# Kernel tuning notes

Measured on AMD Instinct MI355X. Metric: run time of the kernel, lower is better.

## Reference

```python
import jax, jax.numpy as jnp
import numpy as np

VOCAB = 32000
EMB = 1024
BLOCK = 2048
B = 4


def setup_inputs() -> dict:
    key = jax.random.key(0)
    ks = jax.random.split(key, 10)
    s = EMB ** -0.5
    return {
        "idx": jax.random.randint(ks[0], (B, BLOCK), 0, VOCAB),
        "targets": jax.random.randint(ks[1], (B, BLOCK), 0, VOCAB),
        "tok_emb": jax.random.normal(ks[2], (VOCAB, EMB), jnp.float32),
        "pos_emb": jax.random.normal(ks[3], (BLOCK, EMB), jnp.float32),
        "Wk": jax.random.normal(ks[4], (EMB, EMB), jnp.float32) * s,
        "Wq": jax.random.normal(ks[5], (EMB, EMB), jnp.float32) * s,
        "Wv": jax.random.normal(ks[6], (EMB, EMB), jnp.float32) * s,
        "Wlm": jax.random.normal(ks[7], (EMB, VOCAB), jnp.float32) * s,
        "blm": jnp.zeros((VOCAB,), jnp.float32),
    }


def reference(idx, targets, tok_emb, pos_emb, Wk, Wq, Wv, Wlm, blm):
    B_, T = idx.shape
    x = tok_emb[idx] + pos_emb[:T]  # [B,T,C]
    C = x.shape[-1]
    k = x @ Wk  # [B,T,H]
    q = x @ Wq
    v = x @ Wv
    wei = jnp.einsum("bth,bsh->bts", q, k) * (C ** -0.5)  # [B,T,T]
    causal = jnp.tril(jnp.ones((T, T), bool))
    wei = jnp.where(causal, wei, -jnp.inf)
    wei = jax.nn.softmax(wei, axis=-1)
    out = jnp.einsum("bts,bsh->bth", wei, v)  # [B,T,H]
    logits = out @ Wlm + blm  # [B,T,V]
    logits2d = logits.reshape(B_ * T, -1)
    tgt = targets.reshape(B_ * T)
    logp = jax.nn.log_softmax(logits2d, axis=-1)
    loss = -jnp.mean(jnp.take_along_axis(logp, tgt[:, None], axis=1))
    return logits2d, loss
```

## Files before the change

### kernel.cpp

```cpp
#include <hip/hip_runtime.h>
#include <hip/hip_bf16.h>
#include <cstdint>

#define VOCAB 32000
#define EMB   1024
#define TLEN  2048
#define NB    4
#define MTOT  (NB*TLEN)

typedef __bf16 bf16;
typedef __bf16 bf16x8 __attribute__((ext_vector_type(8)));
typedef float  f32x4  __attribute__((ext_vector_type(4)));

__global__ void embed_kernel(const int* __restrict__ idx,
                             const float* __restrict__ tok,
                             const float* __restrict__ pos,
                             bf16* __restrict__ x)
{
    int gid = blockIdx.x * 256 + threadIdx.x;
    int r   = gid >> 7;
    int c0  = (gid & 127) << 3;
    int t   = r & (TLEN - 1);
    int tk  = idx[r];
    const float4* tp = reinterpret_cast<const float4*>(tok + (long)tk * EMB + c0);
    const float4* pp = reinterpret_cast<const float4*>(pos + (long)t  * EMB + c0);
    float4 a0 = tp[0], a1 = tp[1];
    float4 b0 = pp[0], b1 = pp[1];
    bf16x8 o;
    o[0] = (bf16)(a0.x + b0.x); o[1] = (bf16)(a0.y + b0.y);
    o[2] = (bf16)(a0.z + b0.z); o[3] = (bf16)(a0.w + b0.w);
    o[4] = (bf16)(a1.x + b1.x); o[5] = (bf16)(a1.y + b1.y);
    o[6] = (bf16)(a1.z + b1.z); o[7] = (bf16)(a1.w + b1.w);
    *reinterpret_cast<bf16x8*>(x + (long)r * EMB + c0) = o;
}

__global__ void transpose_conv_kernel(const float* __restrict__ W,
                                      bf16* __restrict__ Wt,
                                      int Kdim, int Ndim)
{
    __shared__ bf16 tile[64][65];
    int n0 = blockIdx.x * 64;
    int k0 = blockIdx.y * 64;
    int tid = threadIdx.x;
    int c  = tid & 63, r0 = tid >> 6;
#pragma unroll
    for (int i = 0; i < 16; ++i) {
        int r = r0 + i * 4;
        tile[r][c] = (bf16)W[(long)(k0 + r) * Ndim + n0 + c];
    }
    __syncthreads();
    int kc = tid & 63, nr0 = tid >> 6;
#pragma unroll
    for (int i = 0; i < 16; ++i) {
        int nr = nr0 + i * 4;
        Wt[(long)(n0 + nr) * Kdim + k0 + kc] = tile[kc][nr];
    }
}

__device__ __forceinline__ void gll16(const void* g, void* l)
{
    __builtin_amdgcn_global_load_lds(
        (const __attribute__((address_space(1))) unsigned int*)g,
        (__attribute__((address_space(3))) unsigned int*)l, 16, 0, 0);
}

__device__ __forceinline__ void stage256s(const bf16* __restrict__ gbase,
                                          int ld, int kt, bf16* lbase, int tid)
{
#pragma unroll
    for (int p = 0; p < 4; ++p) {
        int lin  = p * 512 + tid;
        int row  = lin >> 3;
        int slot = lin & 7;
        int ke   = ((slot ^ (row & 7)) << 3) + kt;
        gll16(gbase + (long)row * ld + ke, lbase + lin * 8);
    }
}

template<int CMODE>
__global__ __launch_bounds__(512)
void gemm256_bt(const bf16* __restrict__ A, int lda, long sA,
                const bf16* __restrict__ Bt, int ldb, long sB,
                bf16* __restrict__ C, int ldc, long sC, int K)
{
    if (CMODE == 1 && blockIdx.x > blockIdx.y) return;

    extern __shared__ bf16 smem[];
    bf16* As = smem;
    bf16* Bs = smem + 32768;

    const int tid  = threadIdx.x;
    const int lane = tid & 63, wid = tid >> 6;
    const int wr = wid >> 2, wc = wid & 3;
    const int l15 = lane & 15, hi = lane >> 4, l7 = lane & 7;
    const long zb = blockIdx.z;

    const bf16* Ab = A  + zb * sA + (long)(blockIdx.y * 256) * lda;
    const bf16* Bb = Bt + zb * sB + (long)(blockIdx.x * 256) * ldb;

    const int Keff = (CMODE == 2) ? (int)((blockIdx.y + 1) * 256) : K;
    const int NT   = Keff >> 6;

    f32x4 acc[8][4] = {};

    stage256s(Ab, lda, 0, As, tid);
    stage256s(Bb, ldb, 0, Bs, tid);
    __syncthreads();

#pragma unroll 1
    for (int t = 0; t < NT; ++t) {
        const int buf = t & 1;
        if (t + 1 < NT) {
            stage256s(Ab, lda, (t + 1) * 64, As + (buf ^ 1) * 16384, tid);
            stage256s(Bb, ldb, (t + 1) * 64, Bs + (buf ^ 1) * 16384, tid);
        }
        const bf16* Ap = As + buf * 16384 + (wr * 128) * 64;
        const bf16* Bp = Bs + buf * 16384 + (wc * 64) * 64;
#pragma unroll
        for (int ks = 0; ks < 2; ++ks) {
            const int ko = 8 * (((ks << 2) | hi) ^ l7);
            bf16x8 bfr[4];
#pragma unroll
            for (int n = 0; n < 4; ++n)
                bfr[n] = *(const bf16x8*)(Bp + (n * 16 + l15) * 64 + ko);
#pragma unroll
            for (int m = 0; m < 8; ++m) {
                bf16x8 af = *(const bf16x8*)(Ap + (m * 16 + l15) * 64 + ko);
#pragma unroll
                for (int n = 0; n < 4; ++n)
                    acc[m][n] = __builtin_amdgcn_mfma_f32_16x16x32_bf16(
                                    af, bfr[n], acc[m][n], 0, 0, 0);
            }
        }
        __syncthreads();
    }

    bf16* Cb = C + zb * sC;
    const int colb = blockIdx.x * 256 + wc * 64 + l15;
    const int rowb = blockIdx.y * 256 + wr * 128 + (hi << 2);
#pragma unroll
    for (int m = 0; m < 8; ++m)
#pragma unroll
        for (int n = 0; n < 4; ++n)
#pragma unroll
            for (int r = 0; r < 4; ++r)
                Cb[(long)(rowb + m * 16 + r) * ldc + colb + n * 16] =
                    (bf16)acc[m][n][r];
}

__global__ __launch_bounds__(512)
void gemm256_logits(const bf16* __restrict__ A, const bf16* __restrict__ Bt,
                    float* __restrict__ C, const float* __restrict__ bias,
                    float2* __restrict__ part)
{
    extern __shared__ bf16 smem[];
    bf16* As = smem;
    bf16* Bs = smem + 32768;

    const int tid  = threadIdx.x;
    const int lane = tid & 63, wid = tid >> 6;
    const int wr = wid >> 2, wc = wid & 3;
    const int l15 = lane & 15, hi = lane >> 4, l7 = lane & 7;

    const int wg = blockIdx.x;
    const int xcd = wg & 7, c = wg >> 3;
    const int nb = c >> 2;
    const int mb = xcd * 4 + (c & 3);

    const bf16* Ab = A  + (long)(mb * 256) * EMB;
    const bf16* Bb = Bt + (long)(nb * 256) * EMB;

    f32x4 acc[8][4] = {};

    stage256s(Ab, EMB, 0, As, tid);
    stage256s(Bb, EMB, 0, Bs, tid);
    __syncthreads();

    const int NT = EMB / 64;
#pragma unroll 1
    for (int t = 0; t < NT; ++t) {
        const int buf = t & 1;
        if (t + 1 < NT) {
            stage256s(Ab, EMB, (t + 1) * 64, As + (buf ^ 1) * 16384, tid);
            stage256s(Bb, EMB, (t + 1) * 64, Bs + (buf ^ 1) * 16384, tid);
        }
        const bf16* Ap = As + buf * 16384 + (wr * 128) * 64;
        const bf16* Bp = Bs + buf * 16384 + (wc * 64) * 64;
#pragma unroll
        for (int ks = 0; ks < 2; ++ks) {
            const int ko = 8 * (((ks << 2) | hi) ^ l7);
            bf16x8 bfr[4];
#pragma unroll
            for (int n = 0; n < 4; ++n)
                bfr[n] = *(const bf16x8*)(Bp + (n * 16 + l15) * 64 + ko);
#pragma unroll
            for (int m = 0; m < 8; ++m) {
                bf16x8 af = *(const bf16x8*)(Ap + (m * 16 + l15) * 64 + ko);
#pragma unroll
                for (int n = 0; n < 4; ++n)
                    acc[m][n] = __builtin_amdgcn_mfma_f32_16x16x32_bf16(
                                    af, bfr[n], acc[m][n], 0, 0, 0);
            }
        }
        __syncthreads();
    }

    float* pm = (float*)smem;
    float* ps = pm + 1024;

    const long colbase = (long)nb * 256 + wc * 64 + l15;
    float bv[4];
#pragma unroll
    for (int n = 0; n < 4; ++n) bv[n] = bias[colbase + n * 16];

    const long rowbase = (long)mb * 256 + wr * 128;
#pragma unroll
    for (int m = 0; m < 8; ++m) {
#pragma unroll
        for (int r = 0; r < 4; ++r) {
            float v0 = acc[m][0][r] + bv[0];
            float v1 = acc[m][1][r] + bv[1];
            float v2 = acc[m][2][r] + bv[2];
            float v3 = acc[m][3][r] + bv[3];
            long row = rowbase + m * 16 + (hi << 2) + r;
            float* Cp = C + row * (long)VOCAB + colbase;
            __builtin_nontemporal_store(v0, Cp);
            __builtin_nontemporal_store(v1, Cp + 16);
            __builtin_nontemporal_store(v2, Cp + 32);
            __builtin_nontemporal_store(v3, Cp + 48);

            float lm = fmaxf(fmaxf(v0, v1), fmaxf(v2, v3));
#pragma unroll
            for (int o = 1; o < 16; o <<= 1) lm = fmaxf(lm, __shfl_xor(lm, o));
            float sp = __expf(v0 - lm) + __expf(v1 - lm) +
                       __expf(v2 - lm) + __expf(v3 - lm);
#pragma unroll
            for (int o = 1; o < 16; o <<= 1) sp += __shfl_xor(sp, o);
            if (l15 == 0) {
                int rb = wr * 128 + m * 16 + (hi << 2) + r;
                pm[wc * 256 + rb] = lm;
                ps[wc * 256 + rb] = sp;
            }
        }
    }
    __syncthreads();
    if (tid < 256) {
        float m0 = pm[tid], m1 = pm[256 + tid], m2 = pm[512 + tid], m3 = pm[768 + tid];
        float M = fmaxf(fmaxf(m0, m1), fmaxf(m2, m3));
        float S = ps[tid] * __expf(m0 - M) + ps[256 + tid] * __expf(m1 - M) +
                  ps[512 + tid] * __expf(m2 - M) + ps[768 + tid] * __expf(m3 - M);
        part[((long)mb * 256 + tid) * 125 + nb] = make_float2(M, S);
    }
}

__global__ void softmax_causal_kernel(const bf16* __restrict__ S,
                                      bf16* __restrict__ P)
{
    const int r = blockIdx.x;
    const int t = r & (TLEN - 1);
    const int limit = ((t >> 8) + 1) << 8;
    const int tid = threadIdx.x;
    const int lane = tid & 63, wv = tid >> 6;
    const float scale = 0.03125f;
    const int c0 = tid * 8;

    float v[8];
    float m = -1e30f;
    if (c0 < limit) {
        bf16x8 sv = *(const bf16x8*)(S + (long)r * TLEN + c0);
#pragma unroll
        for (int i = 0; i < 8; ++i) {
            float x = (c0 + i <= t) ? (float)sv[i] * scale : -1e30f;
            v[i] = x;
            m = fmaxf(m, x);
        }
    } else {
#pragma unroll
        for (int i = 0; i < 8; ++i) v[i] = -1e30f;
    }
    __shared__ float red[4];
#pragma unroll
    for (int off = 32; off; off >>= 1) m = fmaxf(m, __shfl_xor(m, off));
    if (lane == 0) red[wv] = m;
    __syncthreads();
    m = fmaxf(fmaxf(red[0], red[1]), fmaxf(red[2], red[3]));
    __syncthreads();

    float s = 0.f;
#pragma unroll
    for (int i = 0; i < 8; ++i) { v[i] = __expf(v[i] - m); s += v[i]; }
#pragma unroll
    for (int off = 32; off; off >>= 1) s += __shfl_xor(s, off);
    if (lane == 0) red[wv] = s;
    __syncthreads();
    s = red[0] + red[1] + red[2] + red[3];
    float inv = 1.0f / s;
    if (c0 < limit) {
        bf16x8 o;
#pragma unroll
        for (int i = 0; i < 8; ++i) o[i] = (bf16)(v[i] * inv);
        *(bf16x8*)(P + (long)r * TLEN + c0) = o;
    }
}

__global__ void loss_combine_kernel(const float2* __restrict__ part,
                                    const float* __restrict__ logits,
                                    const int* __restrict__ tgt,
                                    float* __restrict__ bsum)
{
    const int tid = threadIdx.x;
    const int row = blockIdx.x * 256 + tid;
    const int lane = tid & 63, wv = tid >> 6;
    const float2* p = part + (long)row * 125;
    float M = -1e30f, S = 0.f;
    for (int i = 0; i < 125; ++i) {
        float2 v = p[i];
        if (v.x <= M) S += v.y * __expf(v.x - M);
        else { S = S * __expf(M - v.x) + v.y; M = v.x; }
    }
    float lse = M + __logf(S);
    float l = lse - logits[(long)row * VOCAB + tgt[row]];
#pragma unroll
    for (int off = 32; off; off >>= 1) l += __shfl_xor(l, off);
    __shared__ float red[4];
    if (lane == 0) red[wv] = l;
    __syncthreads();
    if (tid == 0) bsum[blockIdx.x] = red[0] + red[1] + red[2] + red[3];
}

__global__ void loss_final_kernel(const float* __restrict__ bsum,
                                  float* __restrict__ out)
{
    const int lane = threadIdx.x;
    float s = (lane < 32) ? bsum[lane] : 0.f;
#pragma unroll
    for (int off = 32; off; off >>= 1) s += __shfl_xor(s, off);
    if (lane == 0) out[0] = s * (1.0f / MTOT);
}

extern "C" void kernel_launch(void* const* d_in, const int* in_sizes, int n_in,
                              void* d_out, int out_size, void* d_ws, size_t ws_size,
                              hipStream_t stream)
{
    const int*   idx = (const int*)  d_in[0];
    const int*   tgt = (const int*)  d_in[1];
    const float* tok = (const float*)d_in[2];
    const float* pos = (const float*)d_in[3];
    const float* Wk  = (const float*)d_in[4];
    const float* Wq  = (const float*)d_in[5];
    const float* Wv  = (const float*)d_in[6];
    const float* Wlm = (const float*)d_in[7];
    const float* blm = (const float*)d_in[8];
    float* out = (float*)d_out;

    char* ws = (char*)d_ws;
    if (ws_size < (size_t)140 * 1024 * 1024) return;

    bf16*   x     = (bf16*)(ws);
    bf16*   qk    = (bf16*)(ws + (16l << 20));
    bf16*   v_t   = (bf16*)(ws + (48l << 20));
    bf16*   S     = (bf16*)(ws + (64l << 20));
    bf16*   Wqk_t = (bf16*)(ws + (96l << 20));
    bf16*   Wv_t  = (bf16*)(ws + (100l << 20));
    bf16*   att   = (bf16*)(ws);
    bf16*   P     = (bf16*)(ws + (16l << 20));
    bf16*   Wlm_t = (bf16*)(ws + (48l << 20));
    float2* part  = (float2*)(ws + (112l << 20));
    float*  bsum  = (float*)(ws + (120l << 20));

    embed_kernel<<<dim3(MTOT * EMB / 8 / 256), 256, 0, stream>>>(idx, tok, pos, x);

    transpose_conv_kernel<<<dim3(16, 16), 256, 0, stream>>>(Wq, Wqk_t, EMB, EMB);
    transpose_conv_kernel<<<dim3(16, 16), 256, 0, stream>>>(Wk, Wqk_t + 1024 * 1024, EMB, EMB);
    transpose_conv_kernel<<<dim3(16, 16), 256, 0, stream>>>(Wv, Wv_t, EMB, EMB);

    gemm256_bt<0><<<dim3(2048 / 256, MTOT / 256, 1), 512, 131072, stream>>>(
        x, EMB, 0, Wqk_t, EMB, 0, qk, 2048, 0, EMB);
    gemm256_bt<0><<<dim3(MTOT / 256, EMB / 256, 1), 512, 131072, stream>>>(
        Wv_t, EMB, 0, x, EMB, 0, v_t, MTOT, 0, EMB);

    gemm256_bt<1><<<dim3(TLEN / 256, TLEN / 256, NB), 512, 131072, stream>>>(
        qk, 2048, (long)TLEN * 2048, qk + 1024, 2048, (long)TLEN * 2048,
        S, TLEN, (long)TLEN * TLEN, EMB);

    softmax_causal_kernel<<<dim3(MTOT), 256, 0, stream>>>(S, P);

    gemm256_bt<2><<<dim3(EMB / 256, TLEN / 256, NB), 512, 131072, stream>>>(
        P, TLEN, (long)TLEN * TLEN, v_t, MTOT, (long)TLEN,
        att, EMB, (long)TLEN * EMB, TLEN);

    transpose_conv_kernel<<<dim3(VOCAB / 64, EMB / 64), 256, 0, stream>>>(
        Wlm, Wlm_t, EMB, VOCAB);

    gemm256_logits<<<dim3(4000), 512, 131072, stream>>>(att, Wlm_t, out, blm, part);

    loss_combine_kernel<<<dim3(32), 256, 0, stream>>>(part, out, tgt, bsum);
    loss_final_kernel<<<dim3(1), 64, 0, stream>>>(bsum, out + (long)MTOT * VOCAB);
}
```

Before: 847.2 us.

## Co-schedule independent GEMMs and Wlm transpose in combined launches

Merges the V projection GEMM with the causal QK^T score GEMM into one launch, indexing only the lower-triangle tiles directly instead of launching and early-exiting the upper ones. Also merges the causal P·V GEMM with the Wlm transpose/convert into one launch, so the memory-bound transpose blocks fill compute units left idle by the small GEMM grid. Workspace offsets move so Wlm_t no longer aliases v_t while both are live. The cost is branchy heterogeneous blocks that all reserve 128KB of LDS, which limits occupancy for the transpose blocks.

```diff
diff --git a/kernel.cpp b/kernel.cpp
--- a/kernel.cpp
+++ b/kernel.cpp
@@ -78,27 +78,23 @@
 }
 
 template<int CMODE>
-__global__ __launch_bounds__(512)
-void gemm256_bt(const bf16* __restrict__ A, int lda, long sA,
-                const bf16* __restrict__ Bt, int ldb, long sB,
-                bf16* __restrict__ C, int ldc, long sC, int K)
-{
-    if (CMODE == 1 && blockIdx.x > blockIdx.y) return;
-
-    extern __shared__ bf16 smem[];
+__device__ __forceinline__ void gemm256_body(
+    const bf16* __restrict__ A, int lda, long sA,
+    const bf16* __restrict__ Bt, int ldb, long sB,
+    bf16* __restrict__ C, int ldc, long sC, int K,
+    int bx, int by, int zb, bf16* smem, int tid)
+{
     bf16* As = smem;
     bf16* Bs = smem + 32768;
 
-    const int tid  = threadIdx.x;
     const int lane = tid & 63, wid = tid >> 6;
     const int wr = wid >> 2, wc = wid & 3;
     const int l15 = lane & 15, hi = lane >> 4, l7 = lane & 7;
-    const long zb = blockIdx.z;
-
-    const bf16* Ab = A  + zb * sA + (long)(blockIdx.y * 256) * lda;
-    const bf16* Bb = Bt + zb * sB + (long)(blockIdx.x * 256) * ldb;
-
-    const int Keff = (CMODE == 2) ? (int)((blockIdx.y + 1) * 256) : K;
+
+    const bf16* Ab = A  + (long)zb * sA + (long)(by * 256) * lda;
+    const bf16* Bb = Bt + (long)zb * sB + (long)(bx * 256) * ldb;
+
+    const int Keff = (CMODE == 2) ? ((by + 1) * 256) : K;
     const int NT   = Keff >> 6;
 
     f32x4 acc[8][4] = {};
@@ -135,9 +131,9 @@
         __syncthreads();
     }
 
-    bf16* Cb = C + zb * sC;
-    const int colb = blockIdx.x * 256 + wc * 64 + l15;
-    const int rowb = blockIdx.y * 256 + wr * 128 + (hi << 2);
+    bf16* Cb = C + (long)zb * sC;
+    const int colb = bx * 256 + wc * 64 + l15;
+    const int rowb = by * 256 + wr * 128 + (hi << 2);
 #pragma unroll
     for (int m = 0; m < 8; ++m)
 #pragma unroll
@@ -146,6 +142,78 @@
             for (int r = 0; r < 4; ++r)
                 Cb[(long)(rowb + m * 16 + r) * ldc + colb + n * 16] =
                     (bf16)acc[m][n][r];
+}
+
+template<int CMODE>
+__global__ __launch_bounds__(512)
+void gemm256_bt(const bf16* __restrict__ A, int lda, long sA,
+                const bf16* __restrict__ Bt, int ldb, long sB,
+                bf16* __restrict__ C, int ldc, long sC, int K)
+{
+    extern __shared__ bf16 smem[];
+    gemm256_body<CMODE>(A, lda, sA, Bt, ldb, sB, C, ldc, sC, K,
+                        blockIdx.x, blockIdx.y, blockIdx.z, smem, threadIdx.x);
+}
+
+__global__ __launch_bounds__(512)
+void fused_vt_s(const bf16* __restrict__ Wv_t, const bf16* __restrict__ x,
+                bf16* __restrict__ v_t,
+                const bf16* __restrict__ qk, bf16* __restrict__ S)
+{
+    extern __shared__ bf16 smem[];
+    const int q = blockIdx.x, tid = threadIdx.x;
+    if (q < 128) {
+        gemm256_body<0>(Wv_t, EMB, 0, x, EMB, 0, v_t, MTOT, 0, EMB,
+                        q & 31, q >> 5, 0, smem, tid);
+    } else {
+        int q2 = q - 128;
+        int z = q2 / 36, t = q2 % 36;
+        int by = 0, a = 0;
+        while (a + by + 1 <= t) { a += by + 1; ++by; }
+        int bx = t - a;
+        gemm256_body<0>(qk, 2048, (long)TLEN * 2048,
+                        qk + 1024, 2048, (long)TLEN * 2048,
+                        S, TLEN, (long)TLEN * TLEN, EMB, bx, by, z, smem, tid);
+    }
+}
+
+__global__ __launch_bounds__(512)
+void fused_pv_wt(const bf16* __restrict__ P, const bf16* __restrict__ v_t,
+                 bf16* __restrict__ att,
+                 const float* __restrict__ Wlm, bf16* __restrict__ Wlm_t)
+{
+    extern __shared__ bf16 smem[];
+    const int q = blockIdx.x, tid = threadIdx.x;
+    if (q < 128) {
+        gemm256_body<2>(P, TLEN, (long)TLEN * TLEN, v_t, MTOT, (long)TLEN,
+                        att, EMB, (long)TLEN * EMB, TLEN,
+                        q & 3, (q >> 2) & 7, q >> 5, smem, tid);
+    } else {
+        const int q2 = q - 128;
+        const int n0 = (q2 % 125) * 256;
+        const int k0 = (q2 / 125) * 64;
+        bf16 (*tile)[257] = (bf16(*)[257])smem;
+#pragma unroll
+        for (int i = 0; i < 8; ++i) {
+            int lin = i * 512 + tid;
+            int r = lin >> 6, c4 = lin & 63;
+            float4 v = *(const float4*)(Wlm + (long)(k0 + r) * VOCAB + n0 + c4 * 4);
+            tile[r][c4 * 4 + 0] = (bf16)v.x;
+            tile[r][c4 * 4 + 1] = (bf16)v.y;
+            tile[r][c4 * 4 + 2] = (bf16)v.z;
+            tile[r][c4 * 4 + 3] = (bf16)v.w;
+        }
+        __syncthreads();
+#pragma unroll
+        for (int i = 0; i < 4; ++i) {
+            int lin = i * 512 + tid;
+            int nr = lin >> 3, kc8 = (lin & 7) * 8;
+            bf16x8 o;
+#pragma unroll
+            for (int j = 0; j < 8; ++j) o[j] = tile[kc8 + j][nr];
+            *(bf16x8*)(Wlm_t + (long)(n0 + nr) * EMB + k0 + kc8) = o;
+        }
+    }
 }
 
 __global__ __launch_bounds__(512)
@@ -364,9 +432,9 @@
     bf16*   Wv_t  = (bf16*)(ws + (100l << 20));
     bf16*   att   = (bf16*)(ws);
     bf16*   P     = (bf16*)(ws + (16l << 20));
-    bf16*   Wlm_t = (bf16*)(ws + (48l << 20));
-    float2* part  = (float2*)(ws + (112l << 20));
-    float*  bsum  = (float*)(ws + (120l << 20));
+    bf16*   Wlm_t = (bf16*)(ws + (64l << 20));
+    float2* part  = (float2*)(ws + (127l << 20));
+    float*  bsum  = (float*)(ws + (135l << 20));
 
     embed_kernel<<<dim3(MTOT * EMB / 8 / 256), 256, 0, stream>>>(idx, tok, pos, x);
 
@@ -376,21 +444,12 @@
 
     gemm256_bt<0><<<dim3(2048 / 256, MTOT / 256, 1), 512, 131072, stream>>>(
         x, EMB, 0, Wqk_t, EMB, 0, qk, 2048, 0, EMB);
-    gemm256_bt<0><<<dim3(MTOT / 256, EMB / 256, 1), 512, 131072, stream>>>(
-        Wv_t, EMB, 0, x, EMB, 0, v_t, MTOT, 0, EMB);
-
-    gemm256_bt<1><<<dim3(TLEN / 256, TLEN / 256, NB), 512, 131072, stream>>>(
-        qk, 2048, (long)TLEN * 2048, qk + 1024, 2048, (long)TLEN * 2048,
-        S, TLEN, (long)TLEN * TLEN, EMB);
+
+    fused_vt_s<<<dim3(272), 512, 131072, stream>>>(Wv_t, x, v_t, qk, S);
 
     softmax_causal_kernel<<<dim3(MTOT), 256, 0, stream>>>(S, P);
 
-    gemm256_bt<2><<<dim3(EMB / 256, TLEN / 256, NB), 512, 131072, stream>>>(
-        P, TLEN, (long)TLEN * TLEN, v_t, MTOT, (long)TLEN,
-        att, EMB, (long)TLEN * EMB, TLEN);
-
-    transpose_conv_kernel<<<dim3(VOCAB / 64, EMB / 64), 256, 0, stream>>>(
-        Wlm, Wlm_t, EMB, VOCAB);
+    fused_pv_wt<<<dim3(2128), 512, 131072, stream>>>(P, v_t, att, Wlm, Wlm_t);
 
     gemm256_logits<<<dim3(4000), 512, 131072, stream>>>(att, Wlm_t, out, blm, part);
 
```

After: 834.1 us. About the same (-1.5%).
